# Performance work log

Measured on AMD Instinct MI355X. Metric: run time of the kernel, lower is better.

## Reference

```python
import jax, jax.numpy as jnp
import numpy as np

D_MODEL = 768
N_HEADS = 12
D_K = D_MODEL // N_HEADS

def setup_inputs() -> dict:
    key = jax.random.key(0)
    ks = jax.random.split(key, 9)
    B, S = 4, 2048
    s = 1.0 / np.sqrt(D_MODEL)
    return {
        "x": jax.random.normal(ks[0], (B, S, D_MODEL), dtype=jnp.float32),
        "Wq": jax.random.normal(ks[1], (D_MODEL, D_MODEL), dtype=jnp.float32) * s,
        "bq": jnp.zeros((D_MODEL,), dtype=jnp.float32),
        "Wk": jax.random.normal(ks[2], (D_MODEL, D_MODEL), dtype=jnp.float32) * s,
        "bk": jnp.zeros((D_MODEL,), dtype=jnp.float32),
        "Wv": jax.random.normal(ks[3], (D_MODEL, D_MODEL), dtype=jnp.float32) * s,
        "bv": jnp.zeros((D_MODEL,), dtype=jnp.float32),
        "Wo": jax.random.normal(ks[4], (D_MODEL, D_MODEL), dtype=jnp.float32) * s,
        "bo": jnp.zeros((D_MODEL,), dtype=jnp.float32),
    }

def reference(x, Wq, bq, Wk, bk, Wv, bv, Wo, bo):
    B, S, _ = x.shape
    # projections (nn.Linear: x @ W^T + b; here weights stored as (in, out) so x @ W + b)
    q = x @ Wq + bq
    k = x @ Wk + bk
    v = x @ Wv + bv
    # split heads -> (B, H, S, d_k)
    q = q.reshape(B, S, N_HEADS, D_K).transpose(0, 2, 1, 3)
    k = k.reshape(B, S, N_HEADS, D_K).transpose(0, 2, 1, 3)
    v = v.reshape(B, S, N_HEADS, D_K).transpose(0, 2, 1, 3)
    scores = jnp.einsum('bhqd,bhkd->bhqk', q, k) / jnp.sqrt(jnp.float32(D_K))
    causal = jnp.tril(jnp.ones((S, S), dtype=bool))  # True = keep
    scores = jnp.where(causal, scores, jnp.finfo(scores.dtype).min)
    weights = jax.nn.softmax(scores, axis=-1)  # dropout is identity in eval
    out = jnp.einsum('bhqk,bhkd->bhqd', weights, v)
    out = out.transpose(0, 2, 1, 3).reshape(B, S, D_MODEL)
    return out @ Wo + bo
```

## Files before the change

kernel.cpp:

```cpp
#include <hip/hip_runtime.h>
#include <hip/hip_bf16.h>

#define DM    768
#define HEADS 12
#define DK    64
#define SEQ   2048
#define BATCH 4
#define NE    ((size_t)BATCH * SEQ * DM)
#define KT    12
#define BRICK 8192

typedef short v8s __attribute__((ext_vector_type(8)));
typedef float v4f __attribute__((ext_vector_type(4)));

#define LDS_PTR(p) ((__attribute__((address_space(3))) unsigned int*)(p))
#define GLB_PTR(p) ((const __attribute__((address_space(1))) unsigned int*)(p))

__device__ __forceinline__ unsigned short f2bf(float f) {
    union { float f; unsigned u; } v; v.f = f;
    unsigned r = (v.u + 0x7FFFu + ((v.u >> 16) & 1u)) >> 16;
    return (unsigned short)r;
}
__device__ __forceinline__ unsigned short f2bf_trunc(float f) {
    union { float f; unsigned u; } v; v.f = f;
    return (unsigned short)(v.u >> 16);
}

__global__ __launch_bounds__(256)
void cvt_x_kernel(const float* __restrict__ x, unsigned short* __restrict__ xb) {
    const size_t p = ((size_t)blockIdx.x * 256 + threadIdx.x) * 8;
    const int m = (int)(p / DM);
    const int k = (int)(p % DM);
    const float4 a = *(const float4*)(x + p);
    const float4 b = *(const float4*)(x + p + 4);
    v8s o;
    o[0] = (short)f2bf(a.x); o[1] = (short)f2bf(a.y);
    o[2] = (short)f2bf(a.z); o[3] = (short)f2bf(a.w);
    o[4] = (short)f2bf(b.x); o[5] = (short)f2bf(b.y);
    o[6] = (short)f2bf(b.z); o[7] = (short)f2bf(b.w);
    const size_t dst = ((size_t)(m >> 7) * KT + (k >> 6)) * BRICK + (size_t)(m & 127) * 64 + (k & 63);
    *(v8s*)(xb + dst) = o;
}

__global__ __launch_bounds__(256)
void cvt_w_kernel(const float* __restrict__ W0, const float* __restrict__ W1,
                  const float* __restrict__ W2, const float* __restrict__ W3,
                  unsigned short* __restrict__ wt) {
    __shared__ unsigned short T[64][72];
    const int z = blockIdx.z;
    const float* W = (z == 0) ? W0 : (z == 1) ? W1 : (z == 2) ? W2 : W3;
    const float scale = (z == 0) ? 0.125f : 1.0f;
    const int k0 = blockIdx.x * 64, n0 = blockIdx.y * 64;
    const int t = threadIdx.x;
    {
        const int kr = t >> 2;
        const int ns = (t & 3) * 16;
        #pragma unroll
        for (int j = 0; j < 4; ++j) {
            const float4 v = *(const float4*)(W + (size_t)(k0 + kr) * DM + n0 + ns + j * 4);
            T[ns + j * 4 + 0][kr] = f2bf(v.x * scale);
            T[ns + j * 4 + 1][kr] = f2bf(v.y * scale);
            T[ns + j * 4 + 2][kr] = f2bf(v.z * scale);
            T[ns + j * 4 + 3][kr] = f2bf(v.w * scale);
        }
    }
    __syncthreads();
    {
        unsigned short* dst = wt + (size_t)z * DM * DM +
            ((size_t)(n0 >> 7) * KT + (k0 >> 6)) * BRICK + (size_t)(n0 & 64) * 64;
        const int n = t >> 2;
        const int ks = (t & 3) * 16;
        #pragma unroll
        for (int j = 0; j < 2; ++j)
            *(v8s*)(dst + (size_t)n * 64 + ks + j * 8) = *(const v8s*)&T[n][ks + j * 8];
    }
}


__global__ __launch_bounds__(256)
void gemm_qkv_kernel(const unsigned short* __restrict__ xb, const unsigned short* __restrict__ wtbuf,
                     const float* __restrict__ bq, const float* __restrict__ bk,
                     const float* __restrict__ bv,
                     unsigned short* __restrict__ qb, unsigned short* __restrict__ kb,
                     unsigned short* __restrict__ vtb) {
    __shared__ unsigned short smem[16384];
    unsigned short* As = smem;
    unsigned short* Bs = smem + 8192;
    const int z = blockIdx.z;
    const float* bias = (z == 0) ? bq : (z == 1) ? bk : bv;
    const float bscale = (z == 0) ? 0.125f : 1.0f;

    const int t = threadIdx.x;
    const int w = t >> 6, lane = t & 63, quad = lane >> 4, l15 = lane & 15;
    const int wm = w >> 1, wn = w & 1;
    const int M0 = blockIdx.x * 128;
    const int N0 = blockIdx.y * 128;

    const unsigned short* gA = xb + ((size_t)(M0 >> 7) * KT) * BRICK;
    const unsigned short* gB = wtbuf + (size_t)z * DM * DM + ((size_t)(N0 >> 7) * KT) * BRICK;

    const int r8 = lane >> 3;
    const int c8 = (lane & 7) ^ r8;
    const int goff = r8 * 64 + c8 * 8;
    const int rl = l15 & 7, rh = l15 >> 3;

    v4f acc[4][4];
    #pragma unroll
    for (int i = 0; i < 4; ++i)
        #pragma unroll
        for (int j = 0; j < 4; ++j) acc[i][j] = (v4f){0, 0, 0, 0};

    for (int kt = 0; kt < KT; ++kt) {
        const unsigned short* ta = gA + kt * BRICK;
        const unsigned short* tb = gB + kt * BRICK;
        __syncthreads();
        #pragma unroll
        for (int u = 0; u < 4; ++u) {
            const int win = w * 4 + u;
            __builtin_amdgcn_global_load_lds(GLB_PTR(ta + win * 512 + goff), LDS_PTR(As + win * 512), 16, 0, 0);
            __builtin_amdgcn_global_load_lds(GLB_PTR(tb + win * 512 + goff), LDS_PTR(Bs + win * 512), 16, 0, 0);
        }
        __syncthreads();
        #pragma unroll
        for (int kc = 0; kc < 2; ++kc) {
            const int cs = ((kc << 2) | quad) ^ rl;
            v8s a[4], b[4];
            #pragma unroll
            for (int i = 0; i < 4; ++i)
                a[i] = *(const v8s*)&As[(wm * 8 + i * 2 + rh) * 512 + rl * 64 + cs * 8];
            #pragma unroll
            for (int j = 0; j < 4; ++j)
                b[j] = *(const v8s*)&Bs[(wn * 8 + j * 2 + rh) * 512 + rl * 64 + cs * 8];
            #pragma unroll
            for (int i = 0; i < 4; ++i)
                #pragma unroll
                for (int j = 0; j < 4; ++j)
                    acc[i][j] = __builtin_amdgcn_mfma_f32_16x16x32_bf16(a[i], b[j], acc[i][j], 0, 0, 0);
        }
    }

    const int b_ = M0 >> 11;
    const int sidx0 = M0 & 2047;
    const int h0 = N0 >> 6;

    if (z < 2) {
        unsigned short* outp = (z == 0) ? qb : kb;
        #pragma unroll
        for (int j = 0; j < 4; ++j) {
            const int n = N0 + wn * 64 + j * 16 + l15;
            const int h = n >> 6, d = n & 63;
            const float bv_ = bias[n] * bscale;
            #pragma unroll
            for (int i = 0; i < 4; ++i)
                #pragma unroll
                for (int r = 0; r < 4; ++r) {
                    const int sidx = sidx0 + wm * 64 + i * 16 + quad * 4 + r;
                    outp[(((size_t)(b_ * HEADS + h) * SEQ + sidx) << 6) + d] = f2bf(acc[i][j][r] + bv_);
                }
        }
    } else {
        unsigned short* Ts = smem;
        #pragma unroll
        for (int p = 0; p < 2; ++p) {
            __syncthreads();
            if (wm == p) {
                #pragma unroll
                for (int j = 0; j < 4; ++j) {
                    const int dloc = wn * 64 + j * 16 + l15;
                    const float bv_ = bias[N0 + dloc];
                    #pragma unroll
                    for (int i = 0; i < 4; ++i)
                        #pragma unroll
                        for (int r = 0; r < 4; ++r)
                            Ts[dloc * 72 + i * 16 + quad * 4 + r] = f2bf(acc[i][j][r] + bv_);
                }
            }
            __syncthreads();
            const int dloc = t >> 1, ms = (t & 1) * 32;
            const int h = h0 + (dloc >> 6), d = dloc & 63;
            unsigned short* dst = vtb + (((size_t)(b_ * HEADS + h) * DK + d) << 11) + sidx0 + p * 64 + ms;
            #pragma unroll
            for (int jj = 0; jj < 4; ++jj)
                *(v8s*)(dst + jj * 8) = *(const v8s*)&Ts[dloc * 72 + ms + jj * 8];
        }
    }
}

__global__ __launch_bounds__(256)
void gemm_out_kernel(const unsigned short* __restrict__ ob, const unsigned short* __restrict__ wto,
                     const float* __restrict__ bias, float* __restrict__ out) {
    __shared__ unsigned short smem[16384];
    unsigned short* As = smem;
    unsigned short* Bs = smem + 8192;
    const int t = threadIdx.x;
    const int w = t >> 6, lane = t & 63, quad = lane >> 4, l15 = lane & 15;
    const int wm = w >> 1, wn = w & 1;
    const int M0 = blockIdx.x * 128;
    const int N0 = blockIdx.y * 128;

    const unsigned short* gA = ob + ((size_t)(M0 >> 7) * KT) * BRICK;
    const unsigned short* gB = wto + ((size_t)(N0 >> 7) * KT) * BRICK;

    const int r8 = lane >> 3;
    const int c8 = (lane & 7) ^ r8;
    const int goff = r8 * 64 + c8 * 8;
    const int rl = l15 & 7, rh = l15 >> 3;

    v4f acc[4][4];
    #pragma unroll
    for (int i = 0; i < 4; ++i)
        #pragma unroll
        for (int j = 0; j < 4; ++j) acc[i][j] = (v4f){0, 0, 0, 0};

    for (int kt = 0; kt < KT; ++kt) {
        const unsigned short* ta = gA + kt * BRICK;
        const unsigned short* tb = gB + kt * BRICK;
        __syncthreads();
        #pragma unroll
        for (int u = 0; u < 4; ++u) {
            const int win = w * 4 + u;
            __builtin_amdgcn_global_load_lds(GLB_PTR(ta + win * 512 + goff), LDS_PTR(As + win * 512), 16, 0, 0);
            __builtin_amdgcn_global_load_lds(GLB_PTR(tb + win * 512 + goff), LDS_PTR(Bs + win * 512), 16, 0, 0);
        }
        __syncthreads();
        #pragma unroll
        for (int kc = 0; kc < 2; ++kc) {
            const int cs = ((kc << 2) | quad) ^ rl;
            v8s a[4], b[4];
            #pragma unroll
            for (int i = 0; i < 4; ++i)
                a[i] = *(const v8s*)&As[(wm * 8 + i * 2 + rh) * 512 + rl * 64 + cs * 8];
            #pragma unroll
            for (int j = 0; j < 4; ++j)
                b[j] = *(const v8s*)&Bs[(wn * 8 + j * 2 + rh) * 512 + rl * 64 + cs * 8];
            #pragma unroll
            for (int i = 0; i < 4; ++i)
                #pragma unroll
                for (int j = 0; j < 4; ++j)
                    acc[i][j] = __builtin_amdgcn_mfma_f32_16x16x32_bf16(a[i], b[j], acc[i][j], 0, 0, 0);
        }
    }

    #pragma unroll
    for (int j = 0; j < 4; ++j) {
        const int n = N0 + wn * 64 + j * 16 + l15;
        const float bv_ = bias[n];
        #pragma unroll
        for (int i = 0; i < 4; ++i)
            #pragma unroll
            for (int r = 0; r < 4; ++r) {
                const int m = M0 + wm * 64 + i * 16 + quad * 4 + r;
                out[(size_t)m * DM + n] = acc[i][j][r] + bv_;
            }
    }
}

__global__ __launch_bounds__(256)
void attn_kernel(const unsigned short* __restrict__ Q, const unsigned short* __restrict__ K,
                 const unsigned short* __restrict__ VT, unsigned short* __restrict__ O) {
    __shared__ unsigned short Kb[2][64][72];
    __shared__ unsigned short Vb[2][64][72];
    __shared__ unsigned short Ps[4][16][72];
    const int t = threadIdx.x;
    const int w = t >> 6, lane = t & 63, quad = lane >> 4, l15 = lane & 15;

    const int idx = blockIdx.x;
    const int xcd = idx & 7;
    const int j   = idx >> 3;
    const int bh  = xcd + 8 * (j >> 4);
    const int s   = j & 15;
    const int sA  = s, sB = 31 - s;
    const int q0A = sA * 64, q0B = sB * 64;
    const int nkt = sB + 1;
    const size_t kvbase = (size_t)bh * SEQ * DK;

    v8s qfA[2], qfB[2];
    #pragma unroll
    for (int c = 0; c < 2; ++c) {
        qfA[c] = *(const v8s*)(Q + kvbase + (size_t)(q0A + w * 16 + l15) * DK + c * 32 + quad * 8);
        qfB[c] = *(const v8s*)(Q + kvbase + (size_t)(q0B + w * 16 + l15) * DK + c * 32 + quad * 8);
    }

    v4f oA[4], oB[4];
    #pragma unroll
    for (int nf = 0; nf < 4; ++nf) { oA[nf] = (v4f){0,0,0,0}; oB[nf] = (v4f){0,0,0,0}; }
    float lsA[4] = {0,0,0,0}, lsB[4] = {0,0,0,0};

    const int srow = t >> 3;
    const int scol = (t & 7) * 8;

    v8s kr0 = *(const v8s*)(K  + kvbase + (size_t)srow * DK + scol);
    v8s kr1 = *(const v8s*)(K  + kvbase + (size_t)(srow + 32) * DK + scol);
    v8s vr0 = *(const v8s*)(VT + kvbase + ((size_t)srow << 11) + scol);
    v8s vr1 = *(const v8s*)(VT + kvbase + ((size_t)(srow + 32) << 11) + scol);
    *(v8s*)&Kb[0][srow][scol]      = kr0;
    *(v8s*)&Kb[0][srow + 32][scol] = kr1;
    *(v8s*)&Vb[0][srow][scol]      = vr0;
    *(v8s*)&Vb[0][srow + 32][scol] = vr1;
    __syncthreads();

    const int rA = q0A + w * 16 + quad * 4;
    const int rB = q0B + w * 16 + quad * 4;

    for (int kt = 0; kt < nkt; ++kt) {
        const int k0 = kt * 64;
        const int cur = kt & 1;
        if (kt + 1 < nkt) {
            const int kn = k0 + 64;
            kr0 = *(const v8s*)(K  + kvbase + (size_t)(kn + srow) * DK + scol);
            kr1 = *(const v8s*)(K  + kvbase + (size_t)(kn + srow + 32) * DK + scol);
            vr0 = *(const v8s*)(VT + kvbase + ((size_t)srow << 11) + kn + scol);
            vr1 = *(const v8s*)(VT + kvbase + ((size_t)(srow + 32) << 11) + kn + scol);
        }

        {
            v4f sc[4];
            #pragma unroll
            for (int s4 = 0; s4 < 4; ++s4) sc[s4] = (v4f){0,0,0,0};
            #pragma unroll
            for (int c = 0; c < 2; ++c)
                #pragma unroll
                for (int s4 = 0; s4 < 4; ++s4) {
                    const v8s kf = *(const v8s*)&Kb[cur][s4 * 16 + l15][c * 32 + quad * 8];
                    sc[s4] = __builtin_amdgcn_mfma_f32_16x16x32_bf16(qfB[c], kf, sc[s4], 0, 0, 0);
                }
            if (kt < nkt - 1) {
                #pragma unroll
                for (int s4 = 0; s4 < 4; ++s4)
                    #pragma unroll
                    for (int r = 0; r < 4; ++r) {
                        const float p = __expf(sc[s4][r]);
                        lsB[r] += p;
                        Ps[w][quad * 4 + r][s4 * 16 + l15] = f2bf_trunc(p);
                    }
            } else {
                #pragma unroll
                for (int s4 = 0; s4 < 4; ++s4) {
                    const int key = k0 + s4 * 16 + l15;
                    #pragma unroll
                    for (int r = 0; r < 4; ++r) {
                        const float p = (key <= rB + r) ? __expf(sc[s4][r]) : 0.f;
                        lsB[r] += p;
                        Ps[w][quad * 4 + r][s4 * 16 + l15] = f2bf_trunc(p);
                    }
                }
            }
            #pragma unroll
            for (int kc = 0; kc < 2; ++kc) {
                const v8s pf = *(const v8s*)&Ps[w][l15][kc * 32 + quad * 8];
                #pragma unroll
                for (int nf = 0; nf < 4; ++nf) {
                    const v8s vf = *(const v8s*)&Vb[cur][nf * 16 + l15][kc * 32 + quad * 8];
                    oB[nf] = __builtin_amdgcn_mfma_f32_16x16x32_bf16(pf, vf, oB[nf], 0, 0, 0);
                }
            }
        }

        if (kt <= sA) {
            v4f sc[4];
            #pragma unroll
            for (int s4 = 0; s4 < 4; ++s4) sc[s4] = (v4f){0,0,0,0};
            #pragma unroll
            for (int c = 0; c < 2; ++c)
                #pragma unroll
                for (int s4 = 0; s4 < 4; ++s4) {
                    const v8s kf = *(const v8s*)&Kb[cur][s4 * 16 + l15][c * 32 + quad * 8];
                    sc[s4] = __builtin_amdgcn_mfma_f32_16x16x32_bf16(qfA[c], kf, sc[s4], 0, 0, 0);
                }
            if (kt < sA) {
                #pragma unroll
                for (int s4 = 0; s4 < 4; ++s4)
                    #pragma unroll
                    for (int r = 0; r < 4; ++r) {
                        const float p = __expf(sc[s4][r]);
                        lsA[r] += p;
                        Ps[w][quad * 4 + r][s4 * 16 + l15] = f2bf_trunc(p);
                    }
            } else {
                #pragma unroll
                for (int s4 = 0; s4 < 4; ++s4) {
                    const int key = k0 + s4 * 16 + l15;
                    #pragma unroll
                    for (int r = 0; r < 4; ++r) {
                        const float p = (key <= rA + r) ? __expf(sc[s4][r]) : 0.f;
                        lsA[r] += p;
                        Ps[w][quad * 4 + r][s4 * 16 + l15] = f2bf_trunc(p);
                    }
                }
            }
            #pragma unroll
            for (int kc = 0; kc < 2; ++kc) {
                const v8s pf = *(const v8s*)&Ps[w][l15][kc * 32 + quad * 8];
                #pragma unroll
                for (int nf = 0; nf < 4; ++nf) {
                    const v8s vf = *(const v8s*)&Vb[cur][nf * 16 + l15][kc * 32 + quad * 8];
                    oA[nf] = __builtin_amdgcn_mfma_f32_16x16x32_bf16(pf, vf, oA[nf], 0, 0, 0);
                }
            }
        }

        if (kt + 1 < nkt) {
            const int nxt = 1 - cur;
            *(v8s*)&Kb[nxt][srow][scol]      = kr0;
            *(v8s*)&Kb[nxt][srow + 32][scol] = kr1;
            *(v8s*)&Vb[nxt][srow][scol]      = vr0;
            *(v8s*)&Vb[nxt][srow + 32][scol] = vr1;
        }
        __syncthreads();
    }

    #pragma unroll
    for (int off = 1; off < 16; off <<= 1)
        #pragma unroll
        for (int r = 0; r < 4; ++r) {
            lsA[r] += __shfl_xor(lsA[r], off);
            lsB[r] += __shfl_xor(lsB[r], off);
        }

    const int b = bh / HEADS, h = bh % HEADS;
    const size_t brA = ((size_t)(b * 16 + (q0A >> 7)) * KT + h) * BRICK;
    const size_t brB = ((size_t)(b * 16 + (q0B >> 7)) * KT + h) * BRICK;
    #pragma unroll
    for (int r = 0; r < 4; ++r) {
        const float invA = 1.f / lsA[r];
        const float invB = 1.f / lsB[r];
        const int rowlA = (q0A & 127) + w * 16 + quad * 4 + r;
        const int rowlB = (q0B & 127) + w * 16 + quad * 4 + r;
        #pragma unroll
        for (int nf = 0; nf < 4; ++nf) {
            O[brA + (size_t)rowlA * 64 + nf * 16 + l15] = f2bf(oA[nf][r] * invA);
            O[brB + (size_t)rowlB * 64 + nf * 16 + l15] = f2bf(oB[nf][r] * invB);
        }
    }
}

extern "C" void kernel_launch(void* const* d_in, const int* in_sizes, int n_in,
                              void* d_out, int out_size, void* d_ws, size_t ws_size,
                              hipStream_t stream) {
    const float* x  = (const float*)d_in[0];
    const float* Wq = (const float*)d_in[1];
    const float* bq = (const float*)d_in[2];
    const float* Wk = (const float*)d_in[3];
    const float* bk = (const float*)d_in[4];
    const float* Wv = (const float*)d_in[5];
    const float* bv = (const float*)d_in[6];
    const float* Wo = (const float*)d_in[7];
    const float* bo = (const float*)d_in[8];
    float* out = (float*)d_out;

    unsigned short* xb  = (unsigned short*)d_ws;
    unsigned short* qb  = xb  + NE;
    unsigned short* kb  = qb  + NE;
    unsigned short* vtb = kb  + NE;
    unsigned short* wt  = vtb + NE;
    unsigned short* ob  = xb;

    cvt_x_kernel<<<dim3(NE / (8 * 256)), 256, 0, stream>>>(x, xb);
    cvt_w_kernel<<<dim3(12, 12, 4), 256, 0, stream>>>(Wq, Wk, Wv, Wo, wt);
    gemm_qkv_kernel<<<dim3(64, 6, 3), 256, 0, stream>>>(xb, wt, bq, bk, bv, qb, kb, vtb);
    attn_kernel<<<dim3(768), 256, 0, stream>>>(qb, kb, vtb, ob);
    gemm_out_kernel<<<dim3(64, 6), 256, 0, stream>>>(ob, wt + (size_t)3 * DM * DM, bo, out);
}
```

Before: 221.4 us.

## Transpose attention MFMAs, use exp2 with folded scale, narrow out-GEMM tiles

The attention kernel now computes S^T and O^T via swapped MFMA operands. Each lane then owns one query row, so row sums become a single scalar and the cross-lane reduction shrinks to two shuffles. P and O are written as packed uint2 stores. The softmax uses exp2 with log2(e) folded into the Q weight scale, and launch bounds request 3 blocks per CU. Separately, the output GEMM switches to 128x64 tiles to double the block count, and the QKV GEMM grid is flattened to 2D. This trades extra A-tile reloads in the out GEMM for better occupancy and cheaper softmax bookkeeping.

```diff
diff --git a/kernel.cpp b/kernel.cpp
--- a/kernel.cpp
+++ b/kernel.cpp
@@ -21,10 +21,22 @@
     unsigned r = (v.u + 0x7FFFu + ((v.u >> 16) & 1u)) >> 16;
     return (unsigned short)r;
 }
-__device__ __forceinline__ unsigned short f2bf_trunc(float f) {
-    union { float f; unsigned u; } v; v.f = f;
-    return (unsigned short)(v.u >> 16);
-}
+__device__ __forceinline__ unsigned pk2(float a, float b) {
+    union { float f; unsigned u; } x, y; x.f = a; y.f = b;
+    return (x.u >> 16) | (y.u & 0xFFFF0000u);
+}
+__device__ __forceinline__ unsigned pk2r(float a, float b) {
+    return (unsigned)f2bf(a) | ((unsigned)f2bf(b) << 16);
+}
+__device__ __forceinline__ float fexp2(float x) {
+#if __has_builtin(__builtin_amdgcn_exp2f)
+    return __builtin_amdgcn_exp2f(x);
+#else
+    return __expf(x * 0.69314718056f);
+#endif
+}
+
+#define QSCALE 0.18033688011112042f
 
 __global__ __launch_bounds__(256)
 void cvt_x_kernel(const float* __restrict__ x, unsigned short* __restrict__ xb) {
@@ -49,7 +61,7 @@
     __shared__ unsigned short T[64][72];
     const int z = blockIdx.z;
     const float* W = (z == 0) ? W0 : (z == 1) ? W1 : (z == 2) ? W2 : W3;
-    const float scale = (z == 0) ? 0.125f : 1.0f;
+    const float scale = (z == 0) ? QSCALE : 1.0f;
     const int k0 = blockIdx.x * 64, n0 = blockIdx.y * 64;
     const int t = threadIdx.x;
     {
@@ -75,7 +87,6 @@
             *(v8s*)(dst + (size_t)n * 64 + ks + j * 8) = *(const v8s*)&T[n][ks + j * 8];
     }
 }
-
 
 __global__ __launch_bounds__(256)
 void gemm_qkv_kernel(const unsigned short* __restrict__ xb, const unsigned short* __restrict__ wtbuf,
@@ -86,18 +97,19 @@
     __shared__ unsigned short smem[16384];
     unsigned short* As = smem;
     unsigned short* Bs = smem + 8192;
-    const int z = blockIdx.z;
+    const int yb = blockIdx.y;
+    const int z = yb / 6;
+    const int N0 = (yb % 6) * 128;
     const float* bias = (z == 0) ? bq : (z == 1) ? bk : bv;
-    const float bscale = (z == 0) ? 0.125f : 1.0f;
+    const float bscale = (z == 0) ? QSCALE : 1.0f;
 
     const int t = threadIdx.x;
     const int w = t >> 6, lane = t & 63, quad = lane >> 4, l15 = lane & 15;
     const int wm = w >> 1, wn = w & 1;
     const int M0 = blockIdx.x * 128;
-    const int N0 = blockIdx.y * 128;
 
     const unsigned short* gA = xb + ((size_t)(M0 >> 7) * KT) * BRICK;
-    const unsigned short* gB = wtbuf + (size_t)z * DM * DM + ((size_t)(N0 >> 7) * KT) * BRICK;
+    const unsigned short* gB = wtbuf + (size_t)yb * (KT * BRICK);
 
     const int r8 = lane >> 3;
     const int c8 = (lane & 7) ^ r8;
@@ -189,28 +201,28 @@
 __global__ __launch_bounds__(256)
 void gemm_out_kernel(const unsigned short* __restrict__ ob, const unsigned short* __restrict__ wto,
                      const float* __restrict__ bias, float* __restrict__ out) {
-    __shared__ unsigned short smem[16384];
+    __shared__ unsigned short smem[12288];
     unsigned short* As = smem;
     unsigned short* Bs = smem + 8192;
     const int t = threadIdx.x;
     const int w = t >> 6, lane = t & 63, quad = lane >> 4, l15 = lane & 15;
     const int wm = w >> 1, wn = w & 1;
     const int M0 = blockIdx.x * 128;
-    const int N0 = blockIdx.y * 128;
+    const int N0 = blockIdx.y * 64;
 
     const unsigned short* gA = ob + ((size_t)(M0 >> 7) * KT) * BRICK;
-    const unsigned short* gB = wto + ((size_t)(N0 >> 7) * KT) * BRICK;
+    const unsigned short* gB = wto + ((size_t)(N0 >> 7) * KT) * BRICK + (size_t)(N0 & 64) * 64;
 
     const int r8 = lane >> 3;
     const int c8 = (lane & 7) ^ r8;
     const int goff = r8 * 64 + c8 * 8;
     const int rl = l15 & 7, rh = l15 >> 3;
 
-    v4f acc[4][4];
+    v4f acc[4][2];
     #pragma unroll
     for (int i = 0; i < 4; ++i)
         #pragma unroll
-        for (int j = 0; j < 4; ++j) acc[i][j] = (v4f){0, 0, 0, 0};
+        for (int j = 0; j < 2; ++j) acc[i][j] = (v4f){0, 0, 0, 0};
 
     for (int kt = 0; kt < KT; ++kt) {
         const unsigned short* ta = gA + kt * BRICK;
@@ -220,30 +232,34 @@
         for (int u = 0; u < 4; ++u) {
             const int win = w * 4 + u;
             __builtin_amdgcn_global_load_lds(GLB_PTR(ta + win * 512 + goff), LDS_PTR(As + win * 512), 16, 0, 0);
+        }
+        #pragma unroll
+        for (int u = 0; u < 2; ++u) {
+            const int win = w * 2 + u;
             __builtin_amdgcn_global_load_lds(GLB_PTR(tb + win * 512 + goff), LDS_PTR(Bs + win * 512), 16, 0, 0);
         }
         __syncthreads();
         #pragma unroll
         for (int kc = 0; kc < 2; ++kc) {
             const int cs = ((kc << 2) | quad) ^ rl;
-            v8s a[4], b[4];
+            v8s a[4], b[2];
             #pragma unroll
             for (int i = 0; i < 4; ++i)
                 a[i] = *(const v8s*)&As[(wm * 8 + i * 2 + rh) * 512 + rl * 64 + cs * 8];
             #pragma unroll
-            for (int j = 0; j < 4; ++j)
-                b[j] = *(const v8s*)&Bs[(wn * 8 + j * 2 + rh) * 512 + rl * 64 + cs * 8];
+            for (int j = 0; j < 2; ++j)
+                b[j] = *(const v8s*)&Bs[(wn * 4 + j * 2 + rh) * 512 + rl * 64 + cs * 8];
             #pragma unroll
             for (int i = 0; i < 4; ++i)
                 #pragma unroll
-                for (int j = 0; j < 4; ++j)
+                for (int j = 0; j < 2; ++j)
                     acc[i][j] = __builtin_amdgcn_mfma_f32_16x16x32_bf16(a[i], b[j], acc[i][j], 0, 0, 0);
         }
     }
 
     #pragma unroll
-    for (int j = 0; j < 4; ++j) {
-        const int n = N0 + wn * 64 + j * 16 + l15;
+    for (int j = 0; j < 2; ++j) {
+        const int n = N0 + wn * 32 + j * 16 + l15;
         const float bv_ = bias[n];
         #pragma unroll
         for (int i = 0; i < 4; ++i)
@@ -255,7 +271,7 @@
     }
 }
 
-__global__ __launch_bounds__(256)
+__global__ __launch_bounds__(256, 3)
 void attn_kernel(const unsigned short* __restrict__ Q, const unsigned short* __restrict__ K,
                  const unsigned short* __restrict__ VT, unsigned short* __restrict__ O) {
     __shared__ unsigned short Kb[2][64][72];
@@ -284,7 +300,7 @@
     v4f oA[4], oB[4];
     #pragma unroll
     for (int nf = 0; nf < 4; ++nf) { oA[nf] = (v4f){0,0,0,0}; oB[nf] = (v4f){0,0,0,0}; }
-    float lsA[4] = {0,0,0,0}, lsB[4] = {0,0,0,0};
+    float lsA = 0.f, lsB = 0.f;
 
     const int srow = t >> 3;
     const int scol = (t & 7) * 8;
@@ -299,8 +315,8 @@
     *(v8s*)&Vb[0][srow + 32][scol] = vr1;
     __syncthreads();
 
-    const int rA = q0A + w * 16 + quad * 4;
-    const int rB = q0B + w * 16 + quad * 4;
+    const int qA = q0A + w * 16 + l15;
+    const int qB = q0B + w * 16 + l15;
 
     for (int kt = 0; kt < nkt; ++kt) {
         const int k0 = kt * 64;
@@ -313,37 +329,35 @@
             vr1 = *(const v8s*)(VT + kvbase + ((size_t)(srow + 32) << 11) + kn + scol);
         }
 
+        const bool actA = (kt <= sA);
+
+        v4f scB[4], scA[4];
+        #pragma unroll
+        for (int s4 = 0; s4 < 4; ++s4) { scB[s4] = (v4f){0,0,0,0}; scA[s4] = (v4f){0,0,0,0}; }
+        #pragma unroll
+        for (int c = 0; c < 2; ++c)
+            #pragma unroll
+            for (int s4 = 0; s4 < 4; ++s4) {
+                const v8s kf = *(const v8s*)&Kb[cur][s4 * 16 + l15][c * 32 + quad * 8];
+                scB[s4] = __builtin_amdgcn_mfma_f32_16x16x32_bf16(kf, qfB[c], scB[s4], 0, 0, 0);
+                if (actA)
+                    scA[s4] = __builtin_amdgcn_mfma_f32_16x16x32_bf16(kf, qfA[c], scA[s4], 0, 0, 0);
+            }
+
         {
-            v4f sc[4];
-            #pragma unroll
-            for (int s4 = 0; s4 < 4; ++s4) sc[s4] = (v4f){0,0,0,0};
-            #pragma unroll
-            for (int c = 0; c < 2; ++c)
-                #pragma unroll
-                for (int s4 = 0; s4 < 4; ++s4) {
-                    const v8s kf = *(const v8s*)&Kb[cur][s4 * 16 + l15][c * 32 + quad * 8];
-                    sc[s4] = __builtin_amdgcn_mfma_f32_16x16x32_bf16(qfB[c], kf, sc[s4], 0, 0, 0);
-                }
-            if (kt < nkt - 1) {
-                #pragma unroll
-                for (int s4 = 0; s4 < 4; ++s4)
-                    #pragma unroll
-                    for (int r = 0; r < 4; ++r) {
-                        const float p = __expf(sc[s4][r]);
-                        lsB[r] += p;
-                        Ps[w][quad * 4 + r][s4 * 16 + l15] = f2bf_trunc(p);
-                    }
-            } else {
-                #pragma unroll
-                for (int s4 = 0; s4 < 4; ++s4) {
-                    const int key = k0 + s4 * 16 + l15;
-                    #pragma unroll
-                    for (int r = 0; r < 4; ++r) {
-                        const float p = (key <= rB + r) ? __expf(sc[s4][r]) : 0.f;
-                        lsB[r] += p;
-                        Ps[w][quad * 4 + r][s4 * 16 + l15] = f2bf_trunc(p);
-                    }
-                }
+            const bool msk = (kt == nkt - 1);
+            #pragma unroll
+            for (int s4 = 0; s4 < 4; ++s4) {
+                float p[4];
+                #pragma unroll
+                for (int r = 0; r < 4; ++r) {
+                    const int key = k0 + s4 * 16 + quad * 4 + r;
+                    const float e = fexp2(scB[s4][r]);
+                    p[r] = (!msk || key <= qB) ? e : 0.f;
+                    lsB += p[r];
+                }
+                uint2 pkv; pkv.x = pk2(p[0], p[1]); pkv.y = pk2(p[2], p[3]);
+                *(uint2*)&Ps[w][l15][s4 * 16 + quad * 4] = pkv;
             }
             #pragma unroll
             for (int kc = 0; kc < 2; ++kc) {
@@ -351,42 +365,25 @@
                 #pragma unroll
                 for (int nf = 0; nf < 4; ++nf) {
                     const v8s vf = *(const v8s*)&Vb[cur][nf * 16 + l15][kc * 32 + quad * 8];
-                    oB[nf] = __builtin_amdgcn_mfma_f32_16x16x32_bf16(pf, vf, oB[nf], 0, 0, 0);
-                }
-            }
-        }
-
-        if (kt <= sA) {
-            v4f sc[4];
-            #pragma unroll
-            for (int s4 = 0; s4 < 4; ++s4) sc[s4] = (v4f){0,0,0,0};
-            #pragma unroll
-            for (int c = 0; c < 2; ++c)
-                #pragma unroll
-                for (int s4 = 0; s4 < 4; ++s4) {
-                    const v8s kf = *(const v8s*)&Kb[cur][s4 * 16 + l15][c * 32 + quad * 8];
-                    sc[s4] = __builtin_amdgcn_mfma_f32_16x16x32_bf16(qfA[c], kf, sc[s4], 0, 0, 0);
-                }
-            if (kt < sA) {
-                #pragma unroll
-                for (int s4 = 0; s4 < 4; ++s4)
-                    #pragma unroll
-                    for (int r = 0; r < 4; ++r) {
-                        const float p = __expf(sc[s4][r]);
-                        lsA[r] += p;
-                        Ps[w][quad * 4 + r][s4 * 16 + l15] = f2bf_trunc(p);
-                    }
-            } else {
-                #pragma unroll
-                for (int s4 = 0; s4 < 4; ++s4) {
-                    const int key = k0 + s4 * 16 + l15;
-                    #pragma unroll
-                    for (int r = 0; r < 4; ++r) {
-                        const float p = (key <= rA + r) ? __expf(sc[s4][r]) : 0.f;
-                        lsA[r] += p;
-                        Ps[w][quad * 4 + r][s4 * 16 + l15] = f2bf_trunc(p);
-                    }
-                }
+                    oB[nf] = __builtin_amdgcn_mfma_f32_16x16x32_bf16(vf, pf, oB[nf], 0, 0, 0);
+                }
+            }
+        }
+
+        if (actA) {
+            const bool msk = (kt == sA);
+            #pragma unroll
+            for (int s4 = 0; s4 < 4; ++s4) {
+                float p[4];
+                #pragma unroll
+                for (int r = 0; r < 4; ++r) {
+                    const int key = k0 + s4 * 16 + quad * 4 + r;
+                    const float e = fexp2(scA[s4][r]);
+                    p[r] = (!msk || key <= qA) ? e : 0.f;
+                    lsA += p[r];
+                }
+                uint2 pkv; pkv.x = pk2(p[0], p[1]); pkv.y = pk2(p[2], p[3]);
+                *(uint2*)&Ps[w][l15][s4 * 16 + quad * 4] = pkv;
             }
             #pragma unroll
             for (int kc = 0; kc < 2; ++kc) {
@@ -394,7 +391,7 @@
                 #pragma unroll
                 for (int nf = 0; nf < 4; ++nf) {
                     const v8s vf = *(const v8s*)&Vb[cur][nf * 16 + l15][kc * 32 + quad * 8];
-                    oA[nf] = __builtin_amdgcn_mfma_f32_16x16x32_bf16(pf, vf, oA[nf], 0, 0, 0);
+                    oA[nf] = __builtin_amdgcn_mfma_f32_16x16x32_bf16(vf, pf, oA[nf], 0, 0, 0);
                 }
             }
         }
@@ -409,28 +406,24 @@
         __syncthreads();
     }
 
-    #pragma unroll
-    for (int off = 1; off < 16; off <<= 1)
-        #pragma unroll
-        for (int r = 0; r < 4; ++r) {
-            lsA[r] += __shfl_xor(lsA[r], off);
-            lsB[r] += __shfl_xor(lsB[r], off);
-        }
+    lsA += __shfl_xor(lsA, 16); lsA += __shfl_xor(lsA, 32);
+    lsB += __shfl_xor(lsB, 16); lsB += __shfl_xor(lsB, 32);
+    const float invA = 1.f / lsA, invB = 1.f / lsB;
 
     const int b = bh / HEADS, h = bh % HEADS;
     const size_t brA = ((size_t)(b * 16 + (q0A >> 7)) * KT + h) * BRICK;
     const size_t brB = ((size_t)(b * 16 + (q0B >> 7)) * KT + h) * BRICK;
-    #pragma unroll
-    for (int r = 0; r < 4; ++r) {
-        const float invA = 1.f / lsA[r];
-        const float invB = 1.f / lsB[r];
-        const int rowlA = (q0A & 127) + w * 16 + quad * 4 + r;
-        const int rowlB = (q0B & 127) + w * 16 + quad * 4 + r;
-        #pragma unroll
-        for (int nf = 0; nf < 4; ++nf) {
-            O[brA + (size_t)rowlA * 64 + nf * 16 + l15] = f2bf(oA[nf][r] * invA);
-            O[brB + (size_t)rowlB * 64 + nf * 16 + l15] = f2bf(oB[nf][r] * invB);
-        }
+    const int rowlA = (q0A & 127) + w * 16 + l15;
+    const int rowlB = (q0B & 127) + w * 16 + l15;
+    #pragma unroll
+    for (int nf = 0; nf < 4; ++nf) {
+        uint2 a2, b2;
+        a2.x = pk2r(oA[nf][0] * invA, oA[nf][1] * invA);
+        a2.y = pk2r(oA[nf][2] * invA, oA[nf][3] * invA);
+        b2.x = pk2r(oB[nf][0] * invB, oB[nf][1] * invB);
+        b2.y = pk2r(oB[nf][2] * invB, oB[nf][3] * invB);
+        *(uint2*)(O + brA + (size_t)rowlA * 64 + nf * 16 + quad * 4) = a2;
+        *(uint2*)(O + brB + (size_t)rowlB * 64 + nf * 16 + quad * 4) = b2;
     }
 }
 
@@ -457,7 +450,7 @@
 
     cvt_x_kernel<<<dim3(NE / (8 * 256)), 256, 0, stream>>>(x, xb);
     cvt_w_kernel<<<dim3(12, 12, 4), 256, 0, stream>>>(Wq, Wk, Wv, Wo, wt);
-    gemm_qkv_kernel<<<dim3(64, 6, 3), 256, 0, stream>>>(xb, wt, bq, bk, bv, qb, kb, vtb);
+    gemm_qkv_kernel<<<dim3(64, 18), 256, 0, stream>>>(xb, wt, bq, bk, bv, qb, kb, vtb);
     attn_kernel<<<dim3(768), 256, 0, stream>>>(qb, kb, vtb, ob);
-    gemm_out_kernel<<<dim3(64, 6), 256, 0, stream>>>(ob, wt + (size_t)3 * DM * DM, bo, out);
-}
+    gemm_out_kernel<<<dim3(64, 12), 256, 0, stream>>>(ob, wt + (size_t)3 * DM * DM, bo, out);
+}
```

Result: slower. 251.0 us (+13.3%).
